# Optimization experiments

Hardware: AMD Instinct MI355X
Metric: run time of the kernel (lower is better)

## Reference

```python
import jax, jax.numpy as jnp
import numpy as np

N_NODES = 100000
N_EDGES = 400000
N_GRAPHS = 2500
DIM = 128
F_IN = 78
N_LAYERS = 3
BN_EPS = 1e-5


def setup_inputs() -> dict:
    key = jax.random.key(0)
    ks = jax.random.split(key, 24)
    def lin(k, fi, fo):
        return jax.random.normal(k, (fi, fo), jnp.float32) / np.sqrt(fi)
    inp = {
        "x": jax.random.normal(ks[0], (N_NODES, F_IN), jnp.float32),
        "edge_index": jax.random.randint(ks[1], (2, N_EDGES), 0, N_NODES, jnp.int32),
        "batch": jnp.sort(jax.random.randint(ks[2], (N_NODES,), 0, N_GRAPHS, jnp.int32)),
        "num_graphs": N_GRAPHS,
        "gcn1_W": lin(ks[3], F_IN, DIM), "gcn1_b": jnp.zeros((DIM,), jnp.float32),
        "gcn2_W": lin(ks[4], DIM, DIM), "gcn2_b": jnp.zeros((DIM,), jnp.float32),
        "gin0_w1": lin(ks[5], F_IN, DIM), "gin0_b1": jnp.zeros((DIM,), jnp.float32),
        "gin0_w2": lin(ks[6], DIM, DIM), "gin0_b2": jnp.zeros((DIM,), jnp.float32),
        # layers 1..2 stacked (same 128->128 shapes)
        "gin_w1": jnp.stack([lin(ks[7], DIM, DIM), lin(ks[8], DIM, DIM)]),
        "gin_b1": jnp.zeros((2, DIM), jnp.float32),
        "gin_w2": jnp.stack([lin(ks[9], DIM, DIM), lin(ks[10], DIM, DIM)]),
        "gin_b2": jnp.zeros((2, DIM), jnp.float32),
        "bn_gamma": jnp.ones((N_LAYERS, DIM), jnp.float32),
        "bn_beta": jnp.zeros((N_LAYERS, DIM), jnp.float32),
    }
    return inp


def reference(x, edge_index, batch, num_graphs,
              gcn1_W, gcn1_b, gcn2_W, gcn2_b,
              gin0_w1, gin0_b1, gin0_w2, gin0_b2,
              gin_w1, gin_b1, gin_w2, gin_b2,
              bn_gamma, bn_beta):
    n = x.shape[0]
    src, dst = edge_index[0], edge_index[1]

    def gcn(h, W, b):
        # linear -> symmetric-normalized aggregation with self loops (PyG GCNConv)
        h = h @ W
        loop = jnp.arange(n, dtype=src.dtype)
        s = jnp.concatenate([src, loop])
        d = jnp.concatenate([dst, loop])
        deg = jax.ops.segment_sum(jnp.ones(s.shape[0], h.dtype), d, num_segments=n)
        dis = jax.lax.rsqrt(deg)  # deg >= 1 thanks to self loops
        norm = (dis[s] * dis[d])[:, None]
        return jax.ops.segment_sum(h[s] * norm, d, num_segments=n) + b

    def gin(h, w1, b1, w2, b2):
        # GINConv, eps=0: mlp(x + sum_{j->i} x_j)
        agg = jax.ops.segment_sum(h[src], dst, num_segments=n)
        z = jax.nn.relu((h + agg) @ w1 + b1)
        return z @ w2 + b2

    def bn(h, g, bt):
        mu = h.mean(0)
        var = ((h - mu) ** 2).mean(0)
        return (h - mu) * jax.lax.rsqrt(var + BN_EPS) * g + bt

    g1 = jax.nn.relu(gcn(x, gcn1_W, gcn1_b))
    g2 = jax.nn.relu(gcn(g1, gcn2_W, gcn2_b))
    g2a = g2 + g1
    g2m = g2 * g1

    h = x
    xs = []
    m = jnp.float32(1.0)
    e = jnp.float32(0.0)
    for i in range(N_LAYERS):
        if i == 0:
            h = gin(h, gin0_w1, gin0_b1, gin0_w2, gin0_b2)
        else:
            h = gin(h, gin_w1[i - 1], gin_b1[i - 1], gin_w2[i - 1], gin_b2[i - 1])
        h = bn(jax.nn.relu(h), bn_gamma[i], bn_beta[i])
        m = m * h
        e = e + h
        xs.append(h)

    rep = jnp.concatenate(xs + [m, e, g1, g2, g2a, g2m], axis=-1)  # [N, 9*DIM]
    return jax.ops.segment_max(rep, batch, num_segments=num_graphs)
```

## Files before the change

### kernel.cpp

```cpp
#include <hip/hip_runtime.h>
#include <math.h>

#define DIMC 128
#define FINC 78
#define REPW 1152
#define SCAN_TILE 1024

typedef __attribute__((ext_vector_type(8))) short short8x;
typedef __attribute__((ext_vector_type(4))) float f32x4;
typedef unsigned int u32;
typedef const __attribute__((address_space(1))) u32* gas_u32p;
typedef __attribute__((address_space(3))) u32* las_u32p;

__device__ inline float b2f(unsigned short u) {
    union { unsigned int i; float f; } v; v.i = ((unsigned int)u) << 16; return v.f;
}
__device__ inline unsigned short f2b(float f) {
    union { float f; unsigned int i; } v; v.f = f;
    unsigned int r = (v.i + 0x7FFFu + ((v.i >> 16) & 1u)) >> 16;
    return (unsigned short)r;
}

__device__ __forceinline__ void gld16(const void* g, void* l) {
    __builtin_amdgcn_global_load_lds((gas_u32p)g, (las_u32p)l, 16, 0, 0);
}


__global__ void k_fill_int(int* __restrict__ p, int v, int n) {
    int i = blockIdx.x * blockDim.x + threadIdx.x;
    if (i < n) p[i] = v;
}

__global__ void k_fill(float* __restrict__ p, float v, int n) {
    int i = blockIdx.x * blockDim.x + threadIdx.x;
    if (i < n) p[i] = v;
}

__global__ void k_count(const int* __restrict__ dst, int* __restrict__ cnt, int E) {
    int e = blockIdx.x * blockDim.x + threadIdx.x;
    if (e < E) atomicAdd(&cnt[dst[e]], 1);
}

__launch_bounds__(256)
__global__ void k_tilesum(const int* __restrict__ cnt, int* __restrict__ tileSum, int N) {
    __shared__ int red[256];
    int base = blockIdx.x * SCAN_TILE;
    int s = 0;
    for (int i = threadIdx.x; i < SCAN_TILE; i += 256) {
        int idx = base + i;
        if (idx < N) s += cnt[idx];
    }
    red[threadIdx.x] = s;
    __syncthreads();
    for (int d = 128; d > 0; d >>= 1) {
        if (threadIdx.x < d) red[threadIdx.x] += red[threadIdx.x + d];
        __syncthreads();
    }
    if (threadIdx.x == 0) tileSum[blockIdx.x] = red[0];
}

__launch_bounds__(256)
__global__ void k_tilescan(const int* __restrict__ tileSum, int* __restrict__ tileOff,
                           int* __restrict__ rowptr, int T, int N) {
    __shared__ int sh[256];
    int t = threadIdx.x;
    int orig = (t < T) ? tileSum[t] : 0;
    sh[t] = orig;
    __syncthreads();
    for (int d = 1; d < 256; d <<= 1) {
        int v = (t >= d) ? sh[t - d] : 0;
        __syncthreads();
        sh[t] += v;
        __syncthreads();
    }
    if (t < T) tileOff[t] = sh[t] - orig;
    if (t == 255) rowptr[N] = sh[255];
}

__launch_bounds__(256)
__global__ void k_tileemit(const int* __restrict__ cnt, const int* __restrict__ tileOff,
                           int* __restrict__ rowptr, int* __restrict__ cursor,
                           float* __restrict__ dis, int N) {
    __shared__ int sh[256];
    int t = threadIdx.x;
    int base = blockIdx.x * SCAN_TILE;
    int idx0 = base + t * 4;
    int v0 = 0, v1 = 0, v2 = 0, v3 = 0;
    if (idx0 + 3 < N) {
        int4 v = *(const int4*)(cnt + idx0);
        v0 = v.x; v1 = v.y; v2 = v.z; v3 = v.w;
    } else {
        if (idx0 + 0 < N) v0 = cnt[idx0 + 0];
        if (idx0 + 1 < N) v1 = cnt[idx0 + 1];
        if (idx0 + 2 < N) v2 = cnt[idx0 + 2];
        if (idx0 + 3 < N) v3 = cnt[idx0 + 3];
    }
    int s0 = v0, s1 = s0 + v1, s2 = s1 + v2, s3 = s2 + v3;
    sh[t] = s3;
    __syncthreads();
    for (int d = 1; d < 256; d <<= 1) {
        int v = (t >= d) ? sh[t - d] : 0;
        __syncthreads();
        sh[t] += v;
        __syncthreads();
    }
    int gbase = tileOff[blockIdx.x] + ((t == 0) ? 0 : sh[t - 1]);
    int ex[4] = {0, s0, s1, s2};
    int vv[4] = {v0, v1, v2, v3};
#pragma unroll
    for (int j = 0; j < 4; ++j) {
        int idx = idx0 + j;
        if (idx < N) {
            int r = gbase + ex[j];
            rowptr[idx] = r;
            cursor[idx] = r;
            dis[idx] = rsqrtf((float)vv[j] + 1.0f);
        }
    }
}

__global__ void k_scatter(const int* __restrict__ src, const int* __restrict__ dst,
                          int* __restrict__ cursor, int* __restrict__ col, int E) {
    int e = blockIdx.x * blockDim.x + threadIdx.x;
    if (e < E) {
        int pos = atomicAdd(&cursor[dst[e]], 1);
        col[pos] = src[e];
    }
}

__global__ void k_bounds(const int* __restrict__ batch, int* __restrict__ start, int N, int G) {
    int g = blockIdx.x * blockDim.x + threadIdx.x;
    if (g <= G) {
        int lo = 0, hi = N;
        while (lo < hi) { int mid = (lo + hi) >> 1; if (batch[mid] < g) lo = mid + 1; else hi = mid; }
        start[g] = lo;
    }
}


__global__ void k_cvt_w(const float* __restrict__ s0, const float* __restrict__ s1,
                        const float* __restrict__ s2, const float* __restrict__ s3,
                        const float* __restrict__ s4, const float* __restrict__ s5,
                        const float* __restrict__ s6, const float* __restrict__ s7,
                        unsigned short* __restrict__ whi, unsigned short* __restrict__ wlo) {
    int my = blockIdx.y;
    const float* src; int Ksrc, KP; size_t dstoff;
    const size_t o96 = (size_t)128 * 96, o128 = (size_t)128 * 128;
    switch (my) {
        case 0: src = s0; Ksrc = 78;  KP = 96;  dstoff = 0; break;
        case 1: src = s1; Ksrc = 78;  KP = 96;  dstoff = o96; break;
        case 2: src = s2; Ksrc = 128; KP = 128; dstoff = 2 * o96; break;
        case 3: src = s3; Ksrc = 128; KP = 128; dstoff = 2 * o96 + o128; break;
        case 4: src = s4; Ksrc = 128; KP = 128; dstoff = 2 * o96 + 2 * o128; break;
        case 5: src = s5; Ksrc = 128; KP = 128; dstoff = 2 * o96 + 3 * o128; break;
        case 6: src = s6; Ksrc = 128; KP = 128; dstoff = 2 * o96 + 4 * o128; break;
        default: src = s7; Ksrc = 128; KP = 128; dstoff = 2 * o96 + 5 * o128; break;
    }
    int i = blockIdx.x * blockDim.x + threadIdx.x;
    if (i < 128 * KP) {
        int n = i / KP, k = i - n * KP;
        float v = (k < Ksrc) ? src[(size_t)k * DIMC + n] : 0.f;
        unsigned short hi = f2b(v);
        unsigned short lo = f2b(v - b2f(hi));
        whi[dstoff + i] = hi;
        wlo[dstoff + i] = lo;
    }
}


__global__ void k_pad_x(const float* __restrict__ x, float* __restrict__ x96, int N) {
    int i = blockIdx.x * blockDim.x + threadIdx.x;
    int r = i / 24, c4 = (i - r * 24) * 4;
    if (r >= N) return;
    float v[4];
#pragma unroll
    for (int j = 0; j < 4; ++j) { int k = c4 + j; v[j] = (k < FINC) ? x[(size_t)r * FINC + k] : 0.f; }
    *(float4*)(x96 + (size_t)r * 96 + c4) = make_float4(v[0], v[1], v[2], v[3]);
}


template<int KP, bool STATS>
__launch_bounds__(256, 2)
__global__ void k_gemm_c(const float* __restrict__ A,
                         const unsigned short* __restrict__ Bhi,
                         const unsigned short* __restrict__ Blo,
                         const float* __restrict__ bias, const float* __restrict__ rowScale,
                         float* __restrict__ statsOut, float* __restrict__ C,
                         int N, int doRelu) {
    constexpr int NT = KP / 32;
    __shared__ float          ldsA[2][4096];
    __shared__ unsigned short ldsB[2][2][4096];
    __shared__ float sStats[256];
    const int tid = threadIdx.x;
    const int wave = tid >> 6, lane = tid & 63;
    const int lm = lane & 15, q = lane >> 4;
    const int wr = (wave >> 1) * 64, wc = (wave & 1) * 64;
    const int row0 = blockIdx.x * 128;

    const int au = tid & 7, ar = tid >> 3;
    const int bu = tid & 3, br = tid >> 2;

    auto stage = [&](int c, int d) {
        const int cb = c << 5;
#pragma unroll
        for (int p = 0; p < 4; ++p) {
            int r = p * 32 + ar;
            gld16(A + (size_t)(row0 + r) * KP + cb + ((au ^ (r & 7)) << 2),
                  &ldsA[d][(p * 256 + tid) << 2]);
        }
#pragma unroll
        for (int p = 0; p < 2; ++p) {
            int r = p * 64 + br;
            int so = cb + ((bu ^ ((r >> 1) & 3)) << 3);
            gld16(Bhi + (size_t)r * KP + so, &ldsB[d][0][(p * 256 + tid) << 3]);
            gld16(Blo + (size_t)r * KP + so, &ldsB[d][1][(p * 256 + tid) << 3]);
        }
    };

    f32x4 acc[4][4];
#pragma unroll
    for (int a = 0; a < 4; ++a)
#pragma unroll
        for (int b = 0; b < 4; ++b) acc[a][b] = (f32x4){0.f, 0.f, 0.f, 0.f};

    stage(0, 0);
#pragma unroll
    for (int t = 0; t < NT; ++t) {
        const int cur = t & 1;
        if (t + 1 < NT) {
            stage(t + 1, cur ^ 1);
            asm volatile("s_waitcnt vmcnt(8)" ::: "memory");
        } else {
            asm volatile("s_waitcnt vmcnt(0)" ::: "memory");
        }
        __builtin_amdgcn_s_barrier();
        __builtin_amdgcn_sched_barrier(0);

        short8x ah[4], al[4];
#pragma unroll
        for (int rt = 0; rt < 4; ++rt) {
            int m = wr + rt * 16 + lm;
            float4 f0 = *(const float4*)&ldsA[cur][m * 32 + (((2 * q) ^ (m & 7)) << 2)];
            float4 f1 = *(const float4*)&ldsA[cur][m * 32 + ((((2 * q) + 1) ^ (m & 7)) << 2)];
            float ff[8] = {f0.x, f0.y, f0.z, f0.w, f1.x, f1.y, f1.z, f1.w};
#pragma unroll
            for (int j = 0; j < 8; ++j) {
                unsigned short h = f2b(ff[j]);
                ah[rt][j] = (short)h;
                al[rt][j] = (short)f2b(ff[j] - b2f(h));
            }
        }
#pragma unroll
        for (int ct = 0; ct < 4; ++ct) {
            int n = wc + ct * 16 + lm;
            int sl = n * 32 + ((q ^ ((n >> 1) & 3)) << 3);
            short8x bh = *(const short8x*)&ldsB[cur][0][sl];
            short8x bl = *(const short8x*)&ldsB[cur][1][sl];
#pragma unroll
            for (int rt = 0; rt < 4; ++rt) {
                acc[rt][ct] = __builtin_amdgcn_mfma_f32_16x16x32_bf16(bh, ah[rt], acc[rt][ct], 0, 0, 0);
                acc[rt][ct] = __builtin_amdgcn_mfma_f32_16x16x32_bf16(bh, al[rt], acc[rt][ct], 0, 0, 0);
                acc[rt][ct] = __builtin_amdgcn_mfma_f32_16x16x32_bf16(bl, ah[rt], acc[rt][ct], 0, 0, 0);
            }
        }
        __builtin_amdgcn_s_barrier();
    }

    float cs[4][4], cq[4][4];
    if constexpr (STATS) {
#pragma unroll
        for (int a = 0; a < 4; ++a)
#pragma unroll
            for (int b = 0; b < 4; ++b) { cs[a][b] = 0.f; cq[a][b] = 0.f; }
    }

#pragma unroll
    for (int rt = 0; rt < 4; ++rt) {
        int grow = row0 + wr + rt * 16 + lm;
        if (grow < N) {
            float sc = rowScale ? rowScale[grow] : 1.f;
#pragma unroll
            for (int ct = 0; ct < 4; ++ct) {
                int nb = wc + ct * 16 + q * 4;
                float vv[4];
#pragma unroll
                for (int i = 0; i < 4; ++i) {
                    float v = acc[rt][ct][i];
                    if (bias) v += bias[nb + i];
                    if (doRelu) v = fmaxf(v, 0.f);
                    v *= sc;
                    vv[i] = v;
                    if constexpr (STATS) { cs[ct][i] += v; cq[ct][i] = fmaf(v, v, cq[ct][i]); }
                }
                *(float4*)(C + (size_t)grow * DIMC + nb) = make_float4(vv[0], vv[1], vv[2], vv[3]);
            }
        }
    }

    if constexpr (STATS) {
        sStats[tid] = 0.f;
        __syncthreads();
#pragma unroll
        for (int ct = 0; ct < 4; ++ct)
#pragma unroll
            for (int i = 0; i < 4; ++i) {
                float vs = cs[ct][i], vq = cq[ct][i];
#pragma unroll
                for (int o = 1; o < 16; o <<= 1) { vs += __shfl_xor(vs, o); vq += __shfl_xor(vq, o); }
                if (lm == 0) {
                    int colg = wc + ct * 16 + q * 4 + i;
                    atomicAdd(&sStats[colg], vs);
                    atomicAdd(&sStats[DIMC + colg], vq);
                }
            }
        __syncthreads();
        atomicAdd(&statsOut[tid], sStats[tid]);
    }
}


__global__ void k_bn_coef(const float* __restrict__ bnsum, const float* __restrict__ gamma,
                          const float* __restrict__ beta, float* __restrict__ coef, float invN) {
    int c = threadIdx.x;
    float mu  = bnsum[c] * invN;
    float var = bnsum[128 + c] * invN - mu * mu;
    float inv = rsqrtf(var + 1e-5f);
    float s = gamma[c] * inv;
    coef[c] = s;
    coef[128 + c] = beta[c] - mu * s;
}


__global__ void k_fold_w(const float* __restrict__ w1, const float* __restrict__ coefL,
                         unsigned short* __restrict__ fwhi, unsigned short* __restrict__ fwlo,
                         float* __restrict__ cvec) {
    __shared__ float red[128];
    int n = blockIdx.x, k = threadIdx.x;
    float w = w1[(size_t)k * DIMC + n];
    float ws = w * coefL[k];
    unsigned short h = f2b(ws);
    fwhi[(size_t)n * DIMC + k] = h;
    fwlo[(size_t)n * DIMC + k] = f2b(ws - b2f(h));
    red[k] = w * coefL[DIMC + k];
    __syncthreads();
    for (int d = 64; d > 0; d >>= 1) { if (k < d) red[k] += red[k + d]; __syncthreads(); }
    if (k == 0) cvec[n] = red[0];
}


__global__ void k_gather_gcn(const float4* __restrict__ t, const int* __restrict__ rowptr,
                             const int* __restrict__ col, const float* __restrict__ dis,
                             const float4* __restrict__ bias, float4* __restrict__ out, int N) {
    int i = blockIdx.x * blockDim.x + threadIdx.x;
    int node = i >> 5, c4 = i & 31;
    if (node >= N) return;
    int s = rowptr[node], e = rowptr[node + 1];
    float4 acc = t[(size_t)node * 32 + c4];
    for (int k = s; k < e; ++k) {
        float4 v = t[(size_t)col[k] * 32 + c4];
        acc.x += v.x; acc.y += v.y; acc.z += v.z; acc.w += v.w;
    }
    float d = dis[node];
    float4 b = bias[c4];
    float4 o;
    o.x = fmaxf(acc.x * d + b.x, 0.f);
    o.y = fmaxf(acc.y * d + b.y, 0.f);
    o.z = fmaxf(acc.z * d + b.z, 0.f);
    o.w = fmaxf(acc.w * d + b.w, 0.f);
    out[(size_t)node * 32 + c4] = o;
}

__global__ void k_gather_gin(const float4* __restrict__ t, const int* __restrict__ rowptr,
                             const int* __restrict__ col, const float4* __restrict__ bias,
                             float4* __restrict__ out, int N) {
    int i = blockIdx.x * blockDim.x + threadIdx.x;
    int node = i >> 5, c4 = i & 31;
    if (node >= N) return;
    int s = rowptr[node], e = rowptr[node + 1];
    float4 acc = t[(size_t)node * 32 + c4];
    for (int k = s; k < e; ++k) {
        float4 v = t[(size_t)col[k] * 32 + c4];
        acc.x += v.x; acc.y += v.y; acc.z += v.z; acc.w += v.w;
    }
    float4 b = bias[c4];
    float4 o;
    o.x = fmaxf(acc.x + b.x, 0.f);
    o.y = fmaxf(acc.y + b.y, 0.f);
    o.z = fmaxf(acc.z + b.z, 0.f);
    o.w = fmaxf(acc.w + b.w, 0.f);
    out[(size_t)node * 32 + c4] = o;
}


__global__ void k_segmax_gin_all(const float* __restrict__ h0, const float* __restrict__ h1,
                                 const float* __restrict__ h2, const float* __restrict__ coef,
                                 const int* __restrict__ start, float* __restrict__ out) {
    int g = blockIdx.x, c = threadIdx.x;
    float s0 = coef[c],       t0 = coef[128 + c];
    float s1 = coef[256 + c], t1 = coef[384 + c];
    float s2 = coef[512 + c], t2 = coef[640 + c];
    int s = start[g], e = start[g + 1];
    float m0 = -INFINITY, m1 = -INFINITY, m2 = -INFINITY, mm = -INFINITY, me = -INFINITY;
    for (int n = s; n < e; ++n) {
        size_t idx = (size_t)n * DIMC + c;
        float a0 = fmaf(h0[idx], s0, t0);
        float a1 = fmaf(h1[idx], s1, t1);
        float a2 = fmaf(h2[idx], s2, t2);
        m0 = fmaxf(m0, a0); m1 = fmaxf(m1, a1); m2 = fmaxf(m2, a2);
        mm = fmaxf(mm, a0 * a1 * a2);
        me = fmaxf(me, a0 + a1 + a2);
    }
    size_t o = (size_t)g * REPW + c;
    out[o]            = m0;
    out[o + 1 * DIMC] = m1;
    out[o + 2 * DIMC] = m2;
    out[o + 3 * DIMC] = mm;
    out[o + 4 * DIMC] = me;
}

__global__ void k_segmax_gcn(const float* __restrict__ G1, const float* __restrict__ G2,
                             const int* __restrict__ start, float* __restrict__ out) {
    int g = blockIdx.x, c = threadIdx.x;
    int s = start[g], e = start[g + 1];
    float m1 = -INFINITY, m2 = -INFINITY, ma = -INFINITY, mm = -INFINITY;
    for (int n = s; n < e; ++n) {
        float a = G1[(size_t)n * DIMC + c], b = G2[(size_t)n * DIMC + c];
        m1 = fmaxf(m1, a); m2 = fmaxf(m2, b);
        ma = fmaxf(ma, a + b); mm = fmaxf(mm, a * b);
    }
    size_t o = (size_t)g * REPW + c;
    out[o + 5 * DIMC] = m1;
    out[o + 6 * DIMC] = m2;
    out[o + 7 * DIMC] = ma;
    out[o + 8 * DIMC] = mm;
}


extern "C" void kernel_launch(void* const* d_in, const int* in_sizes, int n_in,
                              void* d_out, int out_size, void* d_ws, size_t ws_size,
                              hipStream_t stream) {
    const float* x       = (const float*)d_in[0];
    const int*   ei      = (const int*)d_in[1];
    const int*   batch   = (const int*)d_in[2];
    const float* gcn1_W  = (const float*)d_in[4];
    const float* gcn1_b  = (const float*)d_in[5];
    const float* gcn2_W  = (const float*)d_in[6];
    const float* gcn2_b  = (const float*)d_in[7];
    const float* gin0_w1 = (const float*)d_in[8];
    const float* gin0_b1 = (const float*)d_in[9];
    const float* gin0_w2 = (const float*)d_in[10];
    const float* gin0_b2 = (const float*)d_in[11];
    const float* gin_w1  = (const float*)d_in[12];
    const float* gin_b1  = (const float*)d_in[13];
    const float* gin_w2  = (const float*)d_in[14];
    const float* gin_b2  = (const float*)d_in[15];
    const float* bn_g    = (const float*)d_in[16];
    const float* bn_b    = (const float*)d_in[17];
    float* out = (float*)d_out;

    const int N = in_sizes[0] / FINC;
    const int E = in_sizes[1] / 2;
    const int G = out_size / REPW;
    const int* srcv = ei;
    const int* dstv = ei + E;

    char* ws = (char*)d_ws;
    size_t off = 0;
    auto alloc = [&](size_t bytes) { char* p = ws + off; off += (bytes + 255) & ~(size_t)255; return p; };
    int*   cnt     = (int*)alloc((size_t)N * 4);
    int*   rowptr  = (int*)alloc(((size_t)N + 1) * 4);
    int*   cursor  = (int*)alloc((size_t)N * 4);
    int*   col     = (int*)alloc((size_t)E * 4);
    float* dis     = (float*)alloc((size_t)N * 4);
    float* bnsum   = (float*)alloc(768 * 4);
    float* coef    = (float*)alloc(768 * 4);
    float* cvec    = (float*)alloc(128 * 4);
    int*   start   = (int*)alloc(((size_t)G + 1) * 4);
    int*   tileSum = (int*)alloc(256 * 4);
    int*   tileOff = (int*)alloc(256 * 4);
    const size_t o96 = (size_t)128 * 96, o128 = (size_t)128 * 128;
    const size_t wtElems = 2 * o96 + 6 * o128;
    unsigned short* whi  = (unsigned short*)alloc(wtElems * 2);
    unsigned short* wlo  = (unsigned short*)alloc(wtElems * 2);
    unsigned short* fwhi = (unsigned short*)alloc(o128 * 2);
    unsigned short* fwlo = (unsigned short*)alloc(o128 * 2);
    const size_t fbytes = (size_t)N * DIMC * 4;
    float* bufT = (float*)alloc(fbytes);
    float* bufZ = (float*)alloc(fbytes);
    float* h0   = (float*)alloc(fbytes);
    float* h1   = (float*)alloc(fbytes);
    float* h2   = (float*)alloc(fbytes);
    float* x96  = h1;
    (void)ws_size; (void)n_in;

    const size_t woff[8] = {0, o96, 2 * o96, 2 * o96 + o128, 2 * o96 + 2 * o128,
                            2 * o96 + 3 * o128, 2 * o96 + 4 * o128, 2 * o96 + 5 * o128};

    const int T = 256;
    auto cdiv = [](long a, long b) { return (int)((a + b - 1) / b); };
    const int gemmGrid = cdiv(N, 128);
    const int gatherGrid = cdiv((long)N * 32, T);
    const int nTiles = cdiv(N, SCAN_TILE);
    const float invN = 1.0f / (float)N;

    k_fill_int<<<cdiv(N, T), T, 0, stream>>>(cnt, 0, N);
    k_count<<<cdiv(E, T), T, 0, stream>>>(dstv, cnt, E);
    k_tilesum<<<nTiles, T, 0, stream>>>(cnt, tileSum, N);
    k_tilescan<<<1, T, 0, stream>>>(tileSum, tileOff, rowptr, nTiles, N);
    k_tileemit<<<nTiles, T, 0, stream>>>(cnt, tileOff, rowptr, cursor, dis, N);
    k_scatter<<<cdiv(E, T), T, 0, stream>>>(srcv, dstv, cursor, col, E);
    k_bounds<<<cdiv(G + 1, T), T, 0, stream>>>(batch, start, N, G);
    k_fill<<<3, T, 0, stream>>>(bnsum, 0.f, 768);
    {
        dim3 g(64, 8);
        k_cvt_w<<<g, T, 0, stream>>>(gcn1_W, gin0_w1, gcn2_W, gin0_w2,
                                     gin_w1, gin_w1 + o128, gin_w2, gin_w2 + o128, whi, wlo);
    }
    k_pad_x<<<cdiv((long)N * 24, T), T, 0, stream>>>(x, x96, N);

    k_gemm_c<96, false><<<gemmGrid, T, 0, stream>>>(x96, whi + woff[0], wlo + woff[0],
                                                    nullptr, dis, nullptr, bufT, N, 0);
    k_gather_gcn<<<gatherGrid, T, 0, stream>>>((const float4*)bufT, rowptr, col, dis,
                                               (const float4*)gcn1_b, (float4*)bufZ, N);
    k_gemm_c<128, false><<<gemmGrid, T, 0, stream>>>(bufZ, whi + woff[2], wlo + woff[2],
                                                     nullptr, dis, nullptr, bufT, N, 0);
    k_gather_gcn<<<gatherGrid, T, 0, stream>>>((const float4*)bufT, rowptr, col, dis,
                                               (const float4*)gcn2_b, (float4*)h0, N);
    k_segmax_gcn<<<G, DIMC, 0, stream>>>(bufZ, h0, start, out);

    k_gemm_c<96, false><<<gemmGrid, T, 0, stream>>>(x96, whi + woff[1], wlo + woff[1],
                                                    nullptr, nullptr, nullptr, bufT, N, 0);
    k_gather_gin<<<gatherGrid, T, 0, stream>>>((const float4*)bufT, rowptr, col,
                                               (const float4*)gin0_b1, (float4*)bufZ, N);
    k_gemm_c<128, true><<<gemmGrid, T, 0, stream>>>(bufZ, whi + woff[3], wlo + woff[3],
                                                    gin0_b2, nullptr, bnsum, h0, N, 1);
    k_bn_coef<<<1, DIMC, 0, stream>>>(bnsum, bn_g, bn_b, coef, invN);
    k_fold_w<<<DIMC, DIMC, 0, stream>>>(gin_w1, coef, fwhi, fwlo, cvec);

    k_gemm_c<128, false><<<gemmGrid, T, 0, stream>>>(h0, fwhi, fwlo,
                                                     cvec, nullptr, nullptr, bufT, N, 0);
    k_gather_gin<<<gatherGrid, T, 0, stream>>>((const float4*)bufT, rowptr, col,
                                               (const float4*)gin_b1, (float4*)bufZ, N);
    k_gemm_c<128, true><<<gemmGrid, T, 0, stream>>>(bufZ, whi + woff[6], wlo + woff[6],
                                                    gin_b2, nullptr, bnsum + 256, h1, N, 1);
    k_bn_coef<<<1, DIMC, 0, stream>>>(bnsum + 256, bn_g + DIMC, bn_b + DIMC, coef + 256, invN);
    k_fold_w<<<DIMC, DIMC, 0, stream>>>(gin_w1 + o128, coef + 256, fwhi, fwlo, cvec);

    k_gemm_c<128, false><<<gemmGrid, T, 0, stream>>>(h1, fwhi, fwlo,
                                                     cvec, nullptr, nullptr, bufT, N, 0);
    k_gather_gin<<<gatherGrid, T, 0, stream>>>((const float4*)bufT, rowptr, col,
                                               (const float4*)(gin_b1 + DIMC), (float4*)bufZ, N);
    k_gemm_c<128, true><<<gemmGrid, T, 0, stream>>>(bufZ, whi + woff[7], wlo + woff[7],
                                                    gin_b2 + DIMC, nullptr, bnsum + 512, h2, N, 1);
    k_bn_coef<<<1, DIMC, 0, stream>>>(bnsum + 512, bn_g + 2 * DIMC, bn_b + 2 * DIMC, coef + 512, invN);

    k_segmax_gin_all<<<G, DIMC, 0, stream>>>(h0, h1, h2, coef, start, out);
}
```

Before: 759.6 us.

## Load GEMM A operand directly to registers and preload whole B into LDS

The GEMM no longer stages A tiles through LDS with double buffering. Each lane now reads its A fragments straight from global memory into registers, prefetching one K-chunk ahead. The full B (hi/lo bf16) matrix is loaded into LDS once up front, which removes the per-iteration barriers and LDS traffic for A. In exchange, LDS use grows with K, which can limit occupancy at KP=128, and each lane issues strided global loads for A, which coalesce less well.

```diff
diff --git a/kernel.cpp b/kernel.cpp
--- a/kernel.cpp
+++ b/kernel.cpp
@@ -181,15 +181,14 @@
 
 template<int KP, bool STATS>
 __launch_bounds__(256, 2)
-__global__ void k_gemm_c(const float* __restrict__ A,
+__global__ void k_gemm_r(const float* __restrict__ A,
                          const unsigned short* __restrict__ Bhi,
                          const unsigned short* __restrict__ Blo,
                          const float* __restrict__ bias, const float* __restrict__ rowScale,
                          float* __restrict__ statsOut, float* __restrict__ C,
                          int N, int doRelu) {
     constexpr int NT = KP / 32;
-    __shared__ float          ldsA[2][4096];
-    __shared__ unsigned short ldsB[2][2][4096];
+    __shared__ unsigned short ldsB[NT][2][4096];
     __shared__ float sStats[256];
     const int tid = threadIdx.x;
     const int wave = tid >> 6, lane = tid & 63;
@@ -197,25 +196,36 @@
     const int wr = (wave >> 1) * 64, wc = (wave & 1) * 64;
     const int row0 = blockIdx.x * 128;
 
-    const int au = tid & 7, ar = tid >> 3;
-    const int bu = tid & 3, br = tid >> 2;
-
-    auto stage = [&](int c, int d) {
-        const int cb = c << 5;
-#pragma unroll
-        for (int p = 0; p < 4; ++p) {
-            int r = p * 32 + ar;
-            gld16(A + (size_t)(row0 + r) * KP + cb + ((au ^ (r & 7)) << 2),
-                  &ldsA[d][(p * 256 + tid) << 2]);
-        }
-#pragma unroll
-        for (int p = 0; p < 2; ++p) {
-            int r = p * 64 + br;
-            int so = cb + ((bu ^ ((r >> 1) & 3)) << 3);
-            gld16(Bhi + (size_t)r * KP + so, &ldsB[d][0][(p * 256 + tid) << 3]);
-            gld16(Blo + (size_t)r * KP + so, &ldsB[d][1][(p * 256 + tid) << 3]);
-        }
-    };
+    {
+        const int bu = tid & 3, br = tid >> 2;
+#pragma unroll
+        for (int c = 0; c < NT; ++c) {
+            const int cb = c << 5;
+#pragma unroll
+            for (int p = 0; p < 2; ++p) {
+                int r = p * 64 + br;
+                int so = cb + ((bu ^ ((r >> 1) & 3)) << 3);
+                gld16(Bhi + (size_t)r * KP + so, &ldsB[c][0][(p * 256 + tid) << 3]);
+                gld16(Blo + (size_t)r * KP + so, &ldsB[c][1][(p * 256 + tid) << 3]);
+            }
+        }
+    }
+    asm volatile("s_waitcnt vmcnt(0)" ::: "memory");
+    __syncthreads();
+
+    const float* ap[4];
+#pragma unroll
+    for (int rt = 0; rt < 4; ++rt) {
+        int g = row0 + wr + rt * 16 + lm;
+        ap[rt] = A + (size_t)((g < N) ? g : (N - 1)) * KP + q * 8;
+    }
+
+    float4 c0[4], c1[4], n0[4], n1[4];
+#pragma unroll
+    for (int rt = 0; rt < 4; ++rt) {
+        c0[rt] = *(const float4*)(ap[rt]);
+        c1[rt] = *(const float4*)(ap[rt] + 4);
+    }
 
     f32x4 acc[4][4];
 #pragma unroll
@@ -223,26 +233,20 @@
 #pragma unroll
         for (int b = 0; b < 4; ++b) acc[a][b] = (f32x4){0.f, 0.f, 0.f, 0.f};
 
-    stage(0, 0);
 #pragma unroll
     for (int t = 0; t < NT; ++t) {
-        const int cur = t & 1;
         if (t + 1 < NT) {
-            stage(t + 1, cur ^ 1);
-            asm volatile("s_waitcnt vmcnt(8)" ::: "memory");
-        } else {
-            asm volatile("s_waitcnt vmcnt(0)" ::: "memory");
-        }
-        __builtin_amdgcn_s_barrier();
-        __builtin_amdgcn_sched_barrier(0);
-
+#pragma unroll
+            for (int rt = 0; rt < 4; ++rt) {
+                n0[rt] = *(const float4*)(ap[rt] + (t + 1) * 32);
+                n1[rt] = *(const float4*)(ap[rt] + (t + 1) * 32 + 4);
+            }
+        }
         short8x ah[4], al[4];
 #pragma unroll
         for (int rt = 0; rt < 4; ++rt) {
-            int m = wr + rt * 16 + lm;
-            float4 f0 = *(const float4*)&ldsA[cur][m * 32 + (((2 * q) ^ (m & 7)) << 2)];
-            float4 f1 = *(const float4*)&ldsA[cur][m * 32 + ((((2 * q) + 1) ^ (m & 7)) << 2)];
-            float ff[8] = {f0.x, f0.y, f0.z, f0.w, f1.x, f1.y, f1.z, f1.w};
+            float ff[8] = {c0[rt].x, c0[rt].y, c0[rt].z, c0[rt].w,
+                           c1[rt].x, c1[rt].y, c1[rt].z, c1[rt].w};
 #pragma unroll
             for (int j = 0; j < 8; ++j) {
                 unsigned short h = f2b(ff[j]);
@@ -254,8 +258,8 @@
         for (int ct = 0; ct < 4; ++ct) {
             int n = wc + ct * 16 + lm;
             int sl = n * 32 + ((q ^ ((n >> 1) & 3)) << 3);
-            short8x bh = *(const short8x*)&ldsB[cur][0][sl];
-            short8x bl = *(const short8x*)&ldsB[cur][1][sl];
+            short8x bh = *(const short8x*)&ldsB[t][0][sl];
+            short8x bl = *(const short8x*)&ldsB[t][1][sl];
 #pragma unroll
             for (int rt = 0; rt < 4; ++rt) {
                 acc[rt][ct] = __builtin_amdgcn_mfma_f32_16x16x32_bf16(bh, ah[rt], acc[rt][ct], 0, 0, 0);
@@ -263,7 +267,10 @@
                 acc[rt][ct] = __builtin_amdgcn_mfma_f32_16x16x32_bf16(bl, ah[rt], acc[rt][ct], 0, 0, 0);
             }
         }
-        __builtin_amdgcn_s_barrier();
+        if (t + 1 < NT) {
+#pragma unroll
+            for (int rt = 0; rt < 4; ++rt) { c0[rt] = n0[rt]; c1[rt] = n1[rt]; }
+        }
     }
 
     float cs[4][4], cq[4][4];
@@ -518,39 +525,39 @@
     }
     k_pad_x<<<cdiv((long)N * 24, T), T, 0, stream>>>(x, x96, N);
 
-    k_gemm_c<96, false><<<gemmGrid, T, 0, stream>>>(x96, whi + woff[0], wlo + woff[0],
+    k_gemm_r<96, false><<<gemmGrid, T, 0, stream>>>(x96, whi + woff[0], wlo + woff[0],
                                                     nullptr, dis, nullptr, bufT, N, 0);
     k_gather_gcn<<<gatherGrid, T, 0, stream>>>((const float4*)bufT, rowptr, col, dis,
                                                (const float4*)gcn1_b, (float4*)bufZ, N);
-    k_gemm_c<128, false><<<gemmGrid, T, 0, stream>>>(bufZ, whi + woff[2], wlo + woff[2],
+    k_gemm_r<128, false><<<gemmGrid, T, 0, stream>>>(bufZ, whi + woff[2], wlo + woff[2],
                                                      nullptr, dis, nullptr, bufT, N, 0);
     k_gather_gcn<<<gatherGrid, T, 0, stream>>>((const float4*)bufT, rowptr, col, dis,
                                                (const float4*)gcn2_b, (float4*)h0, N);
     k_segmax_gcn<<<G, DIMC, 0, stream>>>(bufZ, h0, start, out);
 
-    k_gemm_c<96, false><<<gemmGrid, T, 0, stream>>>(x96, whi + woff[1], wlo + woff[1],
+    k_gemm_r<96, false><<<gemmGrid, T, 0, stream>>>(x96, whi + woff[1], wlo + woff[1],
                                                     nullptr, nullptr, nullptr, bufT, N, 0);
     k_gather_gin<<<gatherGrid, T, 0, stream>>>((const float4*)bufT, rowptr, col,
                                                (const float4*)gin0_b1, (float4*)bufZ, N);
-    k_gemm_c<128, true><<<gemmGrid, T, 0, stream>>>(bufZ, whi + woff[3], wlo + woff[3],
+    k_gemm_r<128, true><<<gemmGrid, T, 0, stream>>>(bufZ, whi + woff[3], wlo + woff[3],
                                                     gin0_b2, nullptr, bnsum, h0, N, 1);
     k_bn_coef<<<1, DIMC, 0, stream>>>(bnsum, bn_g, bn_b, coef, invN);
     k_fold_w<<<DIMC, DIMC, 0, stream>>>(gin_w1, coef, fwhi, fwlo, cvec);
 
-    k_gemm_c<128, false><<<gemmGrid, T, 0, stream>>>(h0, fwhi, fwlo,
+    k_gemm_r<128, false><<<gemmGrid, T, 0, stream>>>(h0, fwhi, fwlo,
                                                      cvec, nullptr, nullptr, bufT, N, 0);
     k_gather_gin<<<gatherGrid, T, 0, stream>>>((const float4*)bufT, rowptr, col,
                                                (const float4*)gin_b1, (float4*)bufZ, N);
-    k_gemm_c<128, true><<<gemmGrid, T, 0, stream>>>(bufZ, whi + woff[6], wlo + woff[6],
+    k_gemm_r<128, true><<<gemmGrid, T, 0, stream>>>(bufZ, whi + woff[6], wlo + woff[6],
                                                     gin_b2, nullptr, bnsum + 256, h1, N, 1);
     k_bn_coef<<<1, DIMC, 0, stream>>>(bnsum + 256, bn_g + DIMC, bn_b + DIMC, coef + 256, invN);
     k_fold_w<<<DIMC, DIMC, 0, stream>>>(gin_w1 + o128, coef + 256, fwhi, fwlo, cvec);
 
-    k_gemm_c<128, false><<<gemmGrid, T, 0, stream>>>(h1, fwhi, fwlo,
+    k_gemm_r<128, false><<<gemmGrid, T, 0, stream>>>(h1, fwhi, fwlo,
                                                      cvec, nullptr, nullptr, bufT, N, 0);
     k_gather_gin<<<gatherGrid, T, 0, stream>>>((const float4*)bufT, rowptr, col,
                                                (const float4*)(gin_b1 + DIMC), (float4*)bufZ, N);
-    k_gemm_c<128, true><<<gemmGrid, T, 0, stream>>>(bufZ, whi + woff[7], wlo + woff[7],
+    k_gemm_r<128, true><<<gemmGrid, T, 0, stream>>>(bufZ, whi + woff[7], wlo + woff[7],
                                                     gin_b2 + DIMC, nullptr, bnsum + 512, h2, N, 1);
     k_bn_coef<<<1, DIMC, 0, stream>>>(bnsum + 512, bn_g + 2 * DIMC, bn_b + 2 * DIMC, coef + 512, invN);
 
```

Result: slower. 793.2 us (+4.4%).
